# Kernel tuning notes

Measured on AMD Instinct MI355X. Metric: run time of the kernel, lower is better.

Reference implementation:

```python
import jax, jax.numpy as jnp
import numpy as np

N, P, T, K = 20000, 5, 16, 3
IN, H, O = 150, 64, 128


def setup_inputs() -> dict:
    key = jax.random.key(0)
    k1, k2, k3, k4, k5 = jax.random.split(key, 5)
    x = jax.random.normal(k1, (N, IN), dtype=jnp.float32)
    conn_idx = jax.random.randint(k2, (N, P, T, K), 0, N, dtype=jnp.int32)
    conn_w = jax.random.uniform(k3, (N, P, T, K), dtype=jnp.float32)
    # learned params
    W1 = jax.random.normal(k4, (H, IN), dtype=jnp.float32) * 0.05   # linear_1 (no bias)
    Wg = jax.random.normal(k5, (O, H, P, T), dtype=jnp.float32) * 0.05  # geodesic conv weight
    bg = jnp.zeros((O,), dtype=jnp.float32)                          # geodesic conv bias
    return {"x": x, "conn_idx": conn_idx, "conn_w": conn_w, "W1": W1, "Wg": Wg, "bg": bg}


def reference(x, conn_idx, conn_w, W1, Wg, bg):
    # Linear + ReLU: [N, H]
    h = jax.nn.relu(x @ W1.T)
    # Geodesic patch gather: interpolate vertex features into P x T bins
    g = jnp.take(h, conn_idx, axis=0)                 # [N, P, T, K, H]
    patches = jnp.einsum('nptk,nptkh->npth', conn_w, g)  # [N, P, T, H]
    # Geodesic convolution: contract patch bins and channels
    out = jnp.einsum('npth,ohpt->no', patches, Wg) + bg  # [N, O]
    # L2 normalize per vertex
    norm = jnp.linalg.norm(out, axis=-1, keepdims=True)
    return out / norm
```

## Files before the change

### kernel.cpp

```cpp
#include <hip/hip_runtime.h>
#include <hip/hip_fp16.h>

#define NV   20000
#define KK   3
#define INF  150
#define HH   64
#define OO   128
#define PT   80
#define KTOT 5120
#define NB   80
#define RS   72
#define CB   (NB * RS)
#define XS   168
#define CPS  81

typedef _Float16 fh8 __attribute__((ext_vector_type(8)));
typedef __attribute__((ext_vector_type(4))) float f32x4;
typedef __attribute__((ext_vector_type(8))) unsigned short u16x8;

__device__ __forceinline__ unsigned short f2h(float f) {
    return __half_as_ushort(__float2half(f));
}
__device__ __forceinline__ _Float16 u2h(unsigned short u) {
    union { unsigned short s; _Float16 h; } c; c.s = u; return c.h;
}

__global__ __launch_bounds__(256) void prep_kernel(
    const float* __restrict__ Wg, const float* __restrict__ x,
    const float* __restrict__ W1, unsigned short* __restrict__ W2,
    unsigned short* __restrict__ hb) {
    __shared__ __align__(16) unsigned char smem[32256];
    const int tid = threadIdx.x;

    if (blockIdx.x < 128) {
        float* lds = (float*)smem;
        const int o = blockIdx.x;
        const float* src = Wg + o * KTOT;
        for (int e = tid; e < KTOT / 4; e += 256) {
            const float4 v4 = ((const float4*)src)[e];
            const int t = e * 4;
            const int h = t / 80, bin = t - h * 80;
            lds[h * 81 + bin]     = v4.x;
            lds[h * 81 + bin + 1] = v4.y;
            lds[h * 81 + bin + 2] = v4.z;
            lds[h * 81 + bin + 3] = v4.w;
        }
        __syncthreads();
        for (int e = tid; e < KTOT / 2; e += 256) {
            const int t = e * 2;
            const unsigned int h0 = f2h(lds[(t & 63) * 81 + (t >> 6)]);
            const unsigned int h1 = f2h(lds[((t + 1) & 63) * 81 + ((t + 1) >> 6)]);
            *(unsigned int*)(W2 + (t >> 5) * 4096 + o * 32 + (t & 31)) =
                h0 | (h1 << 16);
        }
        return;
    }

    unsigned short* xs = (unsigned short*)smem;
    unsigned short* ws = xs + 32 * XS;
    const int n0 = (blockIdx.x - 128) * 32;

    {
        const float2* x2 = (const float2*)(x + (size_t)n0 * INF);
        for (int e = tid; e < 32 * (INF / 2); e += 256) {
            const int f = e * 2;
            const int r = f / INF, c = f - r * INF;
            const float2 v = x2[e];
            const unsigned int p =
                (unsigned int)f2h(v.x) | ((unsigned int)f2h(v.y) << 16);
            *(unsigned int*)(xs + r * XS + c) = p;
        }
    }
    for (int e = tid; e < 32 * 9; e += 256) {
        const int r = e / 9, c2 = e - r * 9;
        *(unsigned int*)(xs + r * XS + 150 + c2 * 2) = 0;
    }
    {
        const float2* w2p = (const float2*)W1;
        for (int e = tid; e < 64 * (INF / 2); e += 256) {
            const int f = e * 2;
            const int r = f / INF, c = f - r * INF;
            const float2 v = w2p[e];
            const unsigned int p =
                (unsigned int)f2h(v.x) | ((unsigned int)f2h(v.y) << 16);
            *(unsigned int*)(ws + r * XS + c) = p;
        }
    }
    for (int e = tid; e < 64 * 9; e += 256) {
        const int r = e / 9, c2 = e - r * 9;
        *(unsigned int*)(ws + r * XS + 150 + c2 * 2) = 0;
    }
    __syncthreads();

    const int wv   = tid >> 6;
    const int lane = tid & 63;
    const int q    = lane >> 4;
    const int r16  = lane & 15;
    const int o0   = wv * 16;

    f32x4 acc0 = {0.f, 0.f, 0.f, 0.f};
    f32x4 acc1 = acc0;
    #pragma unroll
    for (int s = 0; s < 5; s++) {
        const int kb = s * 32 + q * 8;
        fh8 a0 = *(const fh8*)(xs + r16 * XS + kb);
        fh8 a1 = *(const fh8*)(xs + (16 + r16) * XS + kb);
        fh8 b  = *(const fh8*)(ws + (o0 + r16) * XS + kb);
        acc0 = __builtin_amdgcn_mfma_f32_16x16x32_f16(a0, b, acc0, 0, 0, 0);
        acc1 = __builtin_amdgcn_mfma_f32_16x16x32_f16(a1, b, acc1, 0, 0, 0);
    }
    #pragma unroll
    for (int r = 0; r < 4; r++) {
        float v0 = acc0[r] > 0.f ? acc0[r] : 0.f;
        float v1 = acc1[r] > 0.f ? acc1[r] : 0.f;
        hb[(n0 + q * 4 + r) * HH + o0 + r16]      = f2h(v0);
        hb[(n0 + 16 + q * 4 + r) * HH + o0 + r16] = f2h(v1);
    }
}

__global__ __launch_bounds__(512, 2) void geo_kernel(
    const int*   __restrict__ conn_idx, const float* __restrict__ conn_w,
    const unsigned short* __restrict__ W2, const unsigned short* __restrict__ hb,
    const float* __restrict__ bg, float* __restrict__ out) {
    __shared__ __align__(16) unsigned short pch[2 * CB];
    __shared__ __align__(16) unsigned short cp[NB * CPS * 8];

    const int tid  = threadIdx.x;
    const int n0   = blockIdx.x * NB;
    const int wv   = tid >> 6;
    const int lane = tid & 63;
    const int q    = lane >> 4;
    const int r16  = lane & 15;
    const int j8   = tid & 7;
    const int v0   = tid >> 3;
    const bool lo  = (v0 < 16);

    for (int e = tid; e < NB * 80; e += 512) {
        const int v = e / 80, cc = e - v * 80;
        const int g = (n0 + v) * (PT * KK) + cc * KK;
        u16x8 pk;
        pk[0] = (unsigned short)conn_idx[g];
        pk[1] = (unsigned short)conn_idx[g + 1];
        pk[2] = (unsigned short)conn_idx[g + 2];
        pk[3] = f2h(conn_w[g]);
        pk[4] = f2h(conn_w[g + 1]);
        pk[5] = f2h(conn_w[g + 2]);
        pk[6] = 0; pk[7] = 0;
        *(u16x8*)(cp + (v * CPS + cc) * 8) = pk;
    }

    f32x4 acc[5];
    #pragma unroll
    for (int m = 0; m < 5; m++) acc[m] = (f32x4){0.f, 0.f, 0.f, 0.f};

    u16x8 pa, pc;
    fh8   hva0, hva1, hva2, hvc0, hvc1, hvc2;

    auto loadg = [&](int cc) {
        pa = *(const u16x8*)(cp + (v0 * CPS + cc) * 8);
        hva0 = *(const fh8*)(hb + (int)pa[0] * HH + j8 * 8);
        hva1 = *(const fh8*)(hb + (int)pa[1] * HH + j8 * 8);
        hva2 = *(const fh8*)(hb + (int)pa[2] * HH + j8 * 8);
        if (lo) {
            pc = *(const u16x8*)(cp + ((v0 + 64) * CPS + cc) * 8);
            hvc0 = *(const fh8*)(hb + (int)pc[0] * HH + j8 * 8);
            hvc1 = *(const fh8*)(hb + (int)pc[1] * HH + j8 * 8);
            hvc2 = *(const fh8*)(hb + (int)pc[2] * HH + j8 * 8);
        }
    };
    auto cwr = [&](unsigned short* buf) {
        const _Float16 a0 = u2h(pa[3]), a1 = u2h(pa[4]), a2 = u2h(pa[5]);
        const fh8 A0 = {a0, a0, a0, a0, a0, a0, a0, a0};
        const fh8 A1 = {a1, a1, a1, a1, a1, a1, a1, a1};
        const fh8 A2 = {a2, a2, a2, a2, a2, a2, a2, a2};
        fh8 ra = hva0 * A0 + hva1 * A1 + hva2 * A2;
        *(fh8*)(buf + v0 * RS + j8 * 8) = ra;
        if (lo) {
            const _Float16 c0 = u2h(pc[3]), c1 = u2h(pc[4]), c2 = u2h(pc[5]);
            const fh8 C0 = {c0, c0, c0, c0, c0, c0, c0, c0};
            const fh8 C1 = {c1, c1, c1, c1, c1, c1, c1, c1};
            const fh8 C2 = {c2, c2, c2, c2, c2, c2, c2, c2};
            fh8 rc = hvc0 * C0 + hvc1 * C1 + hvc2 * C2;
            *(fh8*)(buf + (v0 + 64) * RS + j8 * 8) = rc;
        }
    };
    auto mfmaph = [&](const unsigned short* buf, int cc) {
        const unsigned short* wp =
            W2 + (cc * 2) * 4096 + (wv * 16 + r16) * 32 + q * 8;
        const fh8 bf0 = *(const fh8*)(wp);
        const fh8 bf1 = *(const fh8*)(wp + 4096);
        #pragma unroll
        for (int s = 0; s < 2; s++) {
            const int ao = s * 32 + q * 8;
            const fh8 bf = s ? bf1 : bf0;
            #pragma unroll
            for (int m = 0; m < 5; m++) {
                fh8 af = *(const fh8*)(buf + (m * 16 + r16) * RS + ao);
                acc[m] = __builtin_amdgcn_mfma_f32_16x16x32_f16(af, bf, acc[m], 0, 0, 0);
            }
        }
    };

    __syncthreads();

    loadg(0);
    cwr(pch);
    __syncthreads();

    #pragma unroll 1
    for (int cc = 0; cc < 80; cc++) {
        if (cc + 1 < 80) loadg(cc + 1);
        mfmaph(&pch[(cc & 1) * CB], cc);
        if (cc + 1 < 80) cwr(&pch[((cc + 1) & 1) * CB]);
        __syncthreads();
    }

    float* sums = (float*)pch;
    float* rsy  = sums + NB * 33;

    const float bias = bg[wv * 16 + r16];
    float ps[5][4];
    #pragma unroll
    for (int m = 0; m < 5; m++) {
        f32x4 v = acc[m];
        v[0] += bias; v[1] += bias; v[2] += bias; v[3] += bias;
        acc[m] = v;
        #pragma unroll
        for (int r = 0; r < 4; r++) {
            float s2 = v[r] * v[r];
            s2 += __shfl_xor(s2, 1, 16);
            s2 += __shfl_xor(s2, 2, 16);
            ps[m][r] = s2;
        }
    }
    if ((r16 & 3) == 0) {
        #pragma unroll
        for (int m = 0; m < 5; m++)
            #pragma unroll
            for (int r = 0; r < 4; r++)
                sums[(m * 16 + q * 4 + r) * 33 + wv * 4 + (r16 >> 2)] = ps[m][r];
    }
    __syncthreads();
    if (tid < NB) {
        float tot = 0.f;
        #pragma unroll
        for (int c = 0; c < 32; c++) tot += sums[tid * 33 + c];
        rsy[tid] = rsqrtf(tot);
    }
    __syncthreads();
    #pragma unroll
    for (int m = 0; m < 5; m++) {
        const int rb = n0 + m * 16 + q * 4;
        #pragma unroll
        for (int r = 0; r < 4; r++) {
            const float rs = rsy[m * 16 + q * 4 + r];
            out[(rb + r) * OO + wv * 16 + r16] = acc[m][r] * rs;
        }
    }
}

extern "C" void kernel_launch(void* const* d_in, const int* in_sizes, int n_in,
                              void* d_out, int out_size, void* d_ws, size_t ws_size,
                              hipStream_t stream) {
    const float* x        = (const float*)d_in[0];
    const int*   conn_idx = (const int*)  d_in[1];
    const float* conn_w   = (const float*)d_in[2];
    const float* W1       = (const float*)d_in[3];
    const float* Wg       = (const float*)d_in[4];
    const float* bg       = (const float*)d_in[5];
    float*       out      = (float*)d_out;

    unsigned short* W2    = (unsigned short*)d_ws;
    unsigned short* hb    = W2 + OO * KTOT;

    hipLaunchKernelGGL(prep_kernel, dim3(128 + NV / 32), dim3(256), 0, stream,
                       Wg, x, W1, W2, hb);
    hipLaunchKernelGGL(geo_kernel, dim3(NV / NB), dim3(512), 0, stream,
                       conn_idx, conn_w, W2, hb, bg, out);
}
```

Baseline: 185.7 us.

## Split geodesic conv reduction over bins across two blocks, add normalize kernel

The geo kernel now splits the 80 patch bins into two halves handled by separate blocks, doubling the grid from 250 to 500 blocks. The first half writes fp32 partial outputs, the second writes fp16 partials to workspace. A new norm_kernel adds the partials and bias, then L2-normalizes each row. This aims to fill more CUs on the device at the cost of an extra launch, extra global traffic, and fp16 rounding of one partial sum.

```diff
diff --git a/kernel.cpp b/kernel.cpp
--- a/kernel.cpp
+++ b/kernel.cpp
@@ -12,7 +12,8 @@
 #define RS   72
 #define CB   (NB * RS)
 #define XS   168
-#define CPS  81
+#define NBIN 40
+#define CPS  41
 
 typedef _Float16 fh8 __attribute__((ext_vector_type(8)));
 typedef __attribute__((ext_vector_type(4))) float f32x4;
@@ -20,6 +21,9 @@
 
 __device__ __forceinline__ unsigned short f2h(float f) {
     return __half_as_ushort(__float2half(f));
+}
+__device__ __forceinline__ float h2f(unsigned short u) {
+    return __half2float(__ushort_as_half(u));
 }
 __device__ __forceinline__ _Float16 u2h(unsigned short u) {
     union { unsigned short s; _Float16 h; } c; c.s = u; return c.h;
@@ -121,12 +125,13 @@
 __global__ __launch_bounds__(512, 2) void geo_kernel(
     const int*   __restrict__ conn_idx, const float* __restrict__ conn_w,
     const unsigned short* __restrict__ W2, const unsigned short* __restrict__ hb,
-    const float* __restrict__ bg, float* __restrict__ out) {
+    float* __restrict__ out, unsigned short* __restrict__ parts) {
     __shared__ __align__(16) unsigned short pch[2 * CB];
     __shared__ __align__(16) unsigned short cp[NB * CPS * 8];
 
     const int tid  = threadIdx.x;
-    const int n0   = blockIdx.x * NB;
+    const int ks   = blockIdx.x & 1;
+    const int n0   = (blockIdx.x >> 1) * NB;
     const int wv   = tid >> 6;
     const int lane = tid & 63;
     const int q    = lane >> 4;
@@ -134,10 +139,12 @@
     const int j8   = tid & 7;
     const int v0   = tid >> 3;
     const bool lo  = (v0 < 16);
-
-    for (int e = tid; e < NB * 80; e += 512) {
-        const int v = e / 80, cc = e - v * 80;
-        const int g = (n0 + v) * (PT * KK) + cc * KK;
+    const int bbase = ks * NBIN;
+    const int Sbase = ks * (NBIN * 2);
+
+    for (int e = tid; e < NB * NBIN; e += 512) {
+        const int v = e / NBIN, cc = e - v * NBIN;
+        const int g = (n0 + v) * (PT * KK) + (bbase + cc) * KK;
         u16x8 pk;
         pk[0] = (unsigned short)conn_idx[g];
         pk[1] = (unsigned short)conn_idx[g + 1];
@@ -186,7 +193,7 @@
     };
     auto mfmaph = [&](const unsigned short* buf, int cc) {
         const unsigned short* wp =
-            W2 + (cc * 2) * 4096 + (wv * 16 + r16) * 32 + q * 8;
+            W2 + (Sbase + cc * 2) * 4096 + (wv * 16 + r16) * 32 + q * 8;
         const fh8 bf0 = *(const fh8*)(wp);
         const fh8 bf1 = *(const fh8*)(wp + 4096);
         #pragma unroll
@@ -208,54 +215,74 @@
     __syncthreads();
 
     #pragma unroll 1
-    for (int cc = 0; cc < 80; cc++) {
-        if (cc + 1 < 80) loadg(cc + 1);
+    for (int cc = 0; cc < NBIN; cc++) {
+        if (cc + 1 < NBIN) loadg(cc + 1);
         mfmaph(&pch[(cc & 1) * CB], cc);
-        if (cc + 1 < 80) cwr(&pch[((cc + 1) & 1) * CB]);
+        if (cc + 1 < NBIN) cwr(&pch[((cc + 1) & 1) * CB]);
         __syncthreads();
     }
 
-    float* sums = (float*)pch;
-    float* rsy  = sums + NB * 33;
-
-    const float bias = bg[wv * 16 + r16];
-    float ps[5][4];
-    #pragma unroll
-    for (int m = 0; m < 5; m++) {
-        f32x4 v = acc[m];
-        v[0] += bias; v[1] += bias; v[2] += bias; v[3] += bias;
-        acc[m] = v;
+    if (ks == 0) {
         #pragma unroll
-        for (int r = 0; r < 4; r++) {
-            float s2 = v[r] * v[r];
-            s2 += __shfl_xor(s2, 1, 16);
-            s2 += __shfl_xor(s2, 2, 16);
-            ps[m][r] = s2;
-        }
-    }
-    if ((r16 & 3) == 0) {
-        #pragma unroll
-        for (int m = 0; m < 5; m++)
+        for (int m = 0; m < 5; m++) {
+            const int rb = n0 + m * 16 + q * 4;
             #pragma unroll
             for (int r = 0; r < 4; r++)
-                sums[(m * 16 + q * 4 + r) * 33 + wv * 4 + (r16 >> 2)] = ps[m][r];
-    }
-    __syncthreads();
-    if (tid < NB) {
-        float tot = 0.f;
+                out[(rb + r) * OO + wv * 16 + r16] = acc[m][r];
+        }
+    } else {
         #pragma unroll
-        for (int c = 0; c < 32; c++) tot += sums[tid * 33 + c];
-        rsy[tid] = rsqrtf(tot);
-    }
-    __syncthreads();
-    #pragma unroll
-    for (int m = 0; m < 5; m++) {
-        const int rb = n0 + m * 16 + q * 4;
-        #pragma unroll
-        for (int r = 0; r < 4; r++) {
-            const float rs = rsy[m * 16 + q * 4 + r];
-            out[(rb + r) * OO + wv * 16 + r16] = acc[m][r] * rs;
-        }
+        for (int m = 0; m < 5; m++) {
+            const int rb = n0 + m * 16 + q * 4;
+            #pragma unroll
+            for (int r = 0; r < 4; r++)
+                parts[(rb + r) * OO + wv * 16 + r16] = f2h(acc[m][r]);
+        }
+    }
+}
+
+__global__ __launch_bounds__(256) void norm_kernel(
+    float* __restrict__ out, const unsigned short* __restrict__ parts,
+    const float* __restrict__ bg) {
+    const int tid  = threadIdx.x;
+    const int n    = blockIdx.x * 32 + (tid >> 3);
+    const int l    = tid & 7;
+    const int base = n * OO + l * 16;
+
+    float4 o4[4];
+    #pragma unroll
+    for (int i = 0; i < 4; i++)
+        o4[i] = *(const float4*)(out + base + i * 4);
+
+    u16x8 p0 = *(const u16x8*)(parts + base);
+    u16x8 p1 = *(const u16x8*)(parts + base + 8);
+
+    float4 b4[4];
+    #pragma unroll
+    for (int i = 0; i < 4; i++)
+        b4[i] = *(const float4*)(bg + l * 16 + i * 4);
+
+    float v[16];
+    float s = 0.f;
+    #pragma unroll
+    for (int i = 0; i < 16; i++) {
+        const float ov = (i & 3) == 0 ? o4[i >> 2].x :
+                         (i & 3) == 1 ? o4[i >> 2].y :
+                         (i & 3) == 2 ? o4[i >> 2].z : o4[i >> 2].w;
+        const float bv = (i & 3) == 0 ? b4[i >> 2].x :
+                         (i & 3) == 1 ? b4[i >> 2].y :
+                         (i & 3) == 2 ? b4[i >> 2].z : b4[i >> 2].w;
+        const float pv = h2f((i < 8) ? p0[i] : p1[i & 7]);
+        v[i] = ov + pv + bv;
+        s += v[i] * v[i];
+    }
+    for (int off = 4; off; off >>= 1) s += __shfl_down(s, off, 8);
+    const float r = rsqrtf(__shfl(s, 0, 8));
+    #pragma unroll
+    for (int i = 0; i < 4; i++) {
+        float4 w = {v[i * 4] * r, v[i * 4 + 1] * r,
+                    v[i * 4 + 2] * r, v[i * 4 + 3] * r};
+        *(float4*)(out + base + i * 4) = w;
     }
 }
 
@@ -272,9 +299,12 @@
 
     unsigned short* W2    = (unsigned short*)d_ws;
     unsigned short* hb    = W2 + OO * KTOT;
+    unsigned short* parts = hb + NV * HH;
 
     hipLaunchKernelGGL(prep_kernel, dim3(128 + NV / 32), dim3(256), 0, stream,
                        Wg, x, W1, W2, hb);
-    hipLaunchKernelGGL(geo_kernel, dim3(NV / NB), dim3(512), 0, stream,
-                       conn_idx, conn_w, W2, hb, bg, out);
-}
+    hipLaunchKernelGGL(geo_kernel, dim3(2 * (NV / NB)), dim3(512), 0, stream,
+                       conn_idx, conn_w, W2, hb, out, parts);
+    hipLaunchKernelGGL(norm_kernel, dim3(NV / 32), dim3(256), 0, stream,
+                       out, parts, bg);
+}
```

Result: faster. 158.6 us (median of 2 runs) (-14.6%).

## Split geodesic conv reduction across two blocks per tile with last-block combine

Applied to the files above, without the earlier changes.

Splits the 80 patch bins of each 80-vertex tile across two blocks, so the geo kernel launches 500 blocks instead of 250. Each block writes its partial accumulator to global memory (output or a scratch buffer). The second block to finish, found through an atomic counter, adds the two partials plus the bias and does the L2 normalisation. This targets under-filled CUs on the GPU, since 250 blocks cannot occupy every CU at two blocks each. In exchange it adds a memset, extra global traffic for the partials, and a threadfence/atomic handshake.

```diff
diff --git a/kernel.cpp b/kernel.cpp
--- a/kernel.cpp
+++ b/kernel.cpp
@@ -12,7 +12,8 @@
 #define RS   72
 #define CB   (NB * RS)
 #define XS   168
-#define CPS  81
+#define NBIN 40
+#define CPS  41
 
 typedef _Float16 fh8 __attribute__((ext_vector_type(8)));
 typedef __attribute__((ext_vector_type(4))) float f32x4;
@@ -121,12 +122,16 @@
 __global__ __launch_bounds__(512, 2) void geo_kernel(
     const int*   __restrict__ conn_idx, const float* __restrict__ conn_w,
     const unsigned short* __restrict__ W2, const unsigned short* __restrict__ hb,
-    const float* __restrict__ bg, float* __restrict__ out) {
+    float* __restrict__ out, float* __restrict__ part1,
+    int* __restrict__ cnt, const float* __restrict__ bg) {
     __shared__ __align__(16) unsigned short pch[2 * CB];
     __shared__ __align__(16) unsigned short cp[NB * CPS * 8];
+    __shared__ int isLast;
 
     const int tid  = threadIdx.x;
-    const int n0   = blockIdx.x * NB;
+    const int ks   = blockIdx.x & 1;
+    const int tile = blockIdx.x >> 1;
+    const int n0   = tile * NB;
     const int wv   = tid >> 6;
     const int lane = tid & 63;
     const int q    = lane >> 4;
@@ -134,10 +139,12 @@
     const int j8   = tid & 7;
     const int v0   = tid >> 3;
     const bool lo  = (v0 < 16);
-
-    for (int e = tid; e < NB * 80; e += 512) {
-        const int v = e / 80, cc = e - v * 80;
-        const int g = (n0 + v) * (PT * KK) + cc * KK;
+    const int bbase = ks * NBIN;
+    const int Sbase = ks * (NBIN * 2);
+
+    for (int e = tid; e < NB * NBIN; e += 512) {
+        const int v = e / NBIN, cc = e - v * NBIN;
+        const int g = (n0 + v) * (PT * KK) + (bbase + cc) * KK;
         u16x8 pk;
         pk[0] = (unsigned short)conn_idx[g];
         pk[1] = (unsigned short)conn_idx[g + 1];
@@ -186,7 +193,7 @@
     };
     auto mfmaph = [&](const unsigned short* buf, int cc) {
         const unsigned short* wp =
-            W2 + (cc * 2) * 4096 + (wv * 16 + r16) * 32 + q * 8;
+            W2 + (Sbase + cc * 2) * 4096 + (wv * 16 + r16) * 32 + q * 8;
         const fh8 bf0 = *(const fh8*)(wp);
         const fh8 bf1 = *(const fh8*)(wp + 4096);
         #pragma unroll
@@ -208,26 +215,45 @@
     __syncthreads();
 
     #pragma unroll 1
-    for (int cc = 0; cc < 80; cc++) {
-        if (cc + 1 < 80) loadg(cc + 1);
+    for (int cc = 0; cc < NBIN; cc++) {
+        if (cc + 1 < NBIN) loadg(cc + 1);
         mfmaph(&pch[(cc & 1) * CB], cc);
-        if (cc + 1 < 80) cwr(&pch[((cc + 1) & 1) * CB]);
+        if (cc + 1 < NBIN) cwr(&pch[((cc + 1) & 1) * CB]);
         __syncthreads();
     }
 
+    {
+        float* dst = (ks == 0) ? out : part1;
+        #pragma unroll
+        for (int m = 0; m < 5; m++) {
+            const int rb = n0 + m * 16 + q * 4;
+            #pragma unroll
+            for (int r = 0; r < 4; r++)
+                dst[(rb + r) * OO + wv * 16 + r16] = acc[m][r];
+        }
+    }
+
+    __threadfence();
+    if (tid == 0)
+        isLast = (atomicAdd(&cnt[tile], 1) == 1);
+    __syncthreads();
+    if (!isLast) return;
+    __threadfence();
+
+    const float* other = (ks == 0) ? part1 : out;
     float* sums = (float*)pch;
     float* rsy  = sums + NB * 33;
 
     const float bias = bg[wv * 16 + r16];
+    float v[5][4];
     float ps[5][4];
     #pragma unroll
     for (int m = 0; m < 5; m++) {
-        f32x4 v = acc[m];
-        v[0] += bias; v[1] += bias; v[2] += bias; v[3] += bias;
-        acc[m] = v;
+        const int rb = n0 + m * 16 + q * 4;
         #pragma unroll
         for (int r = 0; r < 4; r++) {
-            float s2 = v[r] * v[r];
+            v[m][r] = other[(rb + r) * OO + wv * 16 + r16] + acc[m][r] + bias;
+            float s2 = v[m][r] * v[m][r];
             s2 += __shfl_xor(s2, 1, 16);
             s2 += __shfl_xor(s2, 2, 16);
             ps[m][r] = s2;
@@ -254,7 +280,7 @@
         #pragma unroll
         for (int r = 0; r < 4; r++) {
             const float rs = rsy[m * 16 + q * 4 + r];
-            out[(rb + r) * OO + wv * 16 + r16] = acc[m][r] * rs;
+            out[(rb + r) * OO + wv * 16 + r16] = v[m][r] * rs;
         }
     }
 }
@@ -272,9 +298,12 @@
 
     unsigned short* W2    = (unsigned short*)d_ws;
     unsigned short* hb    = W2 + OO * KTOT;
-
+    float*          part1 = (float*)(hb + NV * HH);
+    int*            cnt   = (int*)(part1 + NV * OO);
+
+    hipMemsetAsync(cnt, 0, 250 * sizeof(int), stream);
     hipLaunchKernelGGL(prep_kernel, dim3(128 + NV / 32), dim3(256), 0, stream,
                        Wg, x, W1, W2, hb);
-    hipLaunchKernelGGL(geo_kernel, dim3(NV / NB), dim3(512), 0, stream,
-                       conn_idx, conn_w, W2, hb, bg, out);
-}
+    hipLaunchKernelGGL(geo_kernel, dim3(2 * (NV / NB)), dim3(512), 0, stream,
+                       conn_idx, conn_w, W2, hb, out, part1, cnt, bg);
+}
```

After: 358.3 us. 1.93x slower.
